# Kernel optimization log

Measured on AMD Instinct MI355X. Metric: run time of the kernel, lower is better.

The kernel has to match this reference:

```python
import jax, jax.numpy as jnp
import numpy as np

B, T, V = 256, 512, 32
CH, H, HF = 32, 64, 32  # context_hidden, hidden_size, feat-imputation hidden


def setup_inputs() -> dict:
    key = jax.random.key(0)
    ks = iter(jax.random.split(key, 48))
    rn = lambda shape, s=0.05: jax.random.normal(next(ks), shape, jnp.float32) * s
    inp = {
        'values': jax.random.normal(next(ks), (B, T, V), jnp.float32),
        'masks': (jax.random.uniform(next(ks), (B, T, V)) < 0.7).astype(jnp.float32),
        'rain_forward': jax.random.normal(next(ks), (B, T, V), jnp.float32),
        'rain_backward': jax.random.normal(next(ks), (B, T, V), jnp.float32),
        # context_mlp: Linear(3V+1, 2CH) -> ReLU -> Linear(2CH, CH)
        'cmlp_W1': rn((2 * CH, 3 * V + 1)), 'cmlp_b1': rn((2 * CH,)),
        'cmlp_W2': rn((CH, 2 * CH)), 'cmlp_b2': rn((CH,)),
        # GRUCell(3V, CH)
        'gru_Wih': rn((3 * CH, 3 * V)), 'gru_Whh': rn((3 * CH, CH)),
        'gru_bih': rn((3 * CH,)), 'gru_bhh': rn((3 * CH,)),
        # initial_hidden: Linear(2CH, 2H)
        'init_W': rn((2 * H, 2 * CH)), 'init_b': rn((2 * H,)),
        # LSTMCell(2V+2CH, H) forward / backward
        'lstmf_Wih': rn((4 * H, 2 * V + 2 * CH)), 'lstmf_Whh': rn((4 * H, H)),
        'lstmf_bih': rn((4 * H,)), 'lstmf_bhh': rn((4 * H,)),
        'lstmb_Wih': rn((4 * H, 2 * V + 2 * CH)), 'lstmb_Whh': rn((4 * H, H)),
        'lstmb_bih': rn((4 * H,)), 'lstmb_bhh': rn((4 * H,)),
        # recurrent_impute: Linear(2H, V)
        'rimp_W': rn((V, 2 * H)), 'rimp_b': rn((V,)),
        # MLPFeatureImputation
        'feat_W': rn((V, HF, V)), 'feat_b': rn((V, HF)),
        'nl1_W': rn((HF, HF)), 'nl1_b': rn((HF,)),
        'nl2_W': rn((1, HF)), 'nl2_b': rn((1,)),
        # fuse_imputations: Linear(2V, V)
        'fuse_W': rn((V, 2 * V)), 'fuse_b': rn((V,)),
        'lengths': jax.random.randint(next(ks), (B,), T // 2, T + 1).astype(jnp.int32),
    }
    return inp


def _forward(values, masks, rain_forward, rain_backward,
             cmlp_W1, cmlp_b1, cmlp_W2, cmlp_b2,
             gru_Wih, gru_Whh, gru_bih, gru_bhh,
             init_W, init_b,
             lstmf_Wih, lstmf_Whh, lstmf_bih, lstmf_bhh,
             lstmb_Wih, lstmb_Whh, lstmb_bih, lstmb_bhh,
             rimp_W, rimp_b, feat_W, feat_b,
             nl1_W, nl1_b, nl2_W, nl2_b, fuse_W, fuse_b, lengths):
    Bv, Tv, Vv = values.shape
    Hh = lstmf_Whh.shape[1]
    dt = values.dtype

    # padding mask [B,T] -> [B,T,V]
    pm_t = (jnp.arange(Tv)[None, :] < lengths[:, None]).astype(dt)
    padding_masks = jnp.broadcast_to(pm_t[:, :, None], values.shape)

    # summary statistics (faithful to the effective computation in torch forward)
    mask_sum = jnp.maximum(masks.sum(1), 1.0)
    data_means = (masks * values).sum(1) / mask_sum
    diff_sq_sum = ((values - data_means[:, None, :]) ** 2).sum(1)
    data_variance = jnp.where(mask_sum > 1, diff_sq_sum / (mask_sum - 1), 0.0)
    data_stdev = jnp.sqrt(data_variance)
    padding_sum = jnp.maximum(padding_masks.sum(1), 1.0)
    data_missing_rate = 1.0 - masks.sum(1) / padding_sum
    data_stats = jnp.concatenate(
        [lengths[:, None].astype(dt), data_means, data_stdev, data_missing_rate], axis=1)

    # last-observation shift and complement
    x_prime = jnp.concatenate([values[:, :1], values[:, :-1]], axis=1)
    x_comp = (masks * values + (1.0 - masks) * x_prime) * padding_masks

    # context MLP
    hmlp = jax.nn.relu(data_stats @ cmlp_W1.T + cmlp_b1)
    ctx_mlp = hmlp @ cmlp_W2.T + cmlp_b2  # [B,CH]

    # context GRU with per-step padding-masked hn
    gru_in = jnp.concatenate([x_comp, rain_forward, rain_backward], axis=-1)  # [B,T,3V]
    ch = gru_Whh.shape[1]

    def gru_step(carry, xt):
        h, hn = carry
        x, mt = xt
        gi = x @ gru_Wih.T + gru_bih
        gh = h @ gru_Whh.T + gru_bhh
        ir, iz, inn = jnp.split(gi, 3, axis=1)
        hr, hz, hhn = jnp.split(gh, 3, axis=1)
        r = jax.nn.sigmoid(ir + hr)
        z = jax.nn.sigmoid(iz + hz)
        n = jnp.tanh(inn + r * hhn)
        h = (1.0 - z) * n + z * h
        hn = mt[:, None] * h + (1.0 - mt[:, None]) * hn
        return (h, hn), None

    z0 = jnp.zeros((Bv, ch), dt)
    (_, ctx_rnn), _ = jax.lax.scan(gru_step, (z0, z0),
                                   (jnp.swapaxes(gru_in, 0, 1), pm_t.T))

    context_vec = jnp.concatenate([ctx_mlp, ctx_rnn], axis=1)  # [B,2CH]
    h0 = context_vec @ init_W.T + init_b   # [B,2H]
    c0 = jnp.tanh(h0)

    inputs = jnp.concatenate(
        [x_comp, masks, jnp.broadcast_to(context_vec[:, None, :], (Bv, Tv, context_vec.shape[1]))],
        axis=-1)  # [B,T,2V+2CH]
    inp_t = jnp.swapaxes(inputs, 0, 1)  # [T,B,D]

    def lstm_step(Wih, Whh, bih, bhh):
        def step(carry, x):
            h, c = carry
            g = x @ Wih.T + bih + h @ Whh.T + bhh
            i, f, gg, o = jnp.split(g, 4, axis=1)
            c = jax.nn.sigmoid(f) * c + jax.nn.sigmoid(i) * jnp.tanh(gg)
            h = jax.nn.sigmoid(o) * jnp.tanh(c)
            return (h, c), h
        return step

    h0f, h0b = h0[:, :Hh], h0[:, Hh:]
    c0f, c0b = c0[:, :Hh], c0[:, Hh:]

    # forward pass over steps 0..T-2; hiddens_forward[0] is initial state
    _, hs_f = jax.lax.scan(lstm_step(lstmf_Wih, lstmf_Whh, lstmf_bih, lstmf_bhh),
                           (h0f, c0f), inp_t[:-1])
    hiddens_forward = jnp.concatenate([h0f[None], hs_f], axis=0)  # [T,B,H]

    # backward pass over steps T-1..1; hiddens_backward[T-1] is initial state
    _, hs_b = jax.lax.scan(lstm_step(lstmb_Wih, lstmb_Whh, lstmb_bih, lstmb_bhh),
                           (h0b, c0b), jnp.flip(inp_t[1:], axis=0))
    hiddens_backward = jnp.concatenate([jnp.flip(hs_b, axis=0), h0b[None]], axis=0)

    rnn_hidden = jnp.swapaxes(
        jnp.concatenate([hiddens_forward, hiddens_backward], axis=2), 0, 1)  # [B,T,2H]
    rnn_imp = rnn_hidden @ rimp_W.T + rimp_b  # [B,T,V]

    # per-variable masked feature imputation
    m = 1.0 - jnp.eye(Vv, dtype=dt)[:, None, :]           # [V,1,V] -> zero own feature
    Wm = feat_W * m                                        # [V,HF,V]
    hid = jnp.einsum('btv,ihv->btih', x_comp, Wm) + feat_b # [B,T,V,HF]
    zh = jax.nn.relu(hid) @ nl1_W.T + nl1_b
    feat_imp = (jax.nn.relu(zh) @ nl2_W.T + nl2_b)[..., 0] # [B,T,V]

    gamma = jnp.ones_like(x_comp)
    beta = jax.nn.sigmoid(jnp.concatenate([gamma, masks], axis=-1) @ fuse_W.T + fuse_b)
    imp_fusion = beta * feat_imp + (1.0 - beta) * rnn_imp
    final_imp = masks * values + (1.0 - masks) * imp_fusion
    final_imp = jnp.where(padding_masks == 1.0, final_imp, 0.0)  # rescale()
    return final_imp


def reference(values, masks, rain_forward, rain_backward,
              cmlp_W1, cmlp_b1, cmlp_W2, cmlp_b2,
              gru_Wih, gru_Whh, gru_bih, gru_bhh,
              init_W, init_b,
              lstmf_Wih, lstmf_Whh, lstmf_bih, lstmf_bhh,
              lstmb_Wih, lstmb_Whh, lstmb_bih, lstmb_bhh,
              rimp_W, rimp_b, feat_W, feat_b,
              nl1_W, nl1_b, nl2_W, nl2_b, fuse_W, fuse_b, lengths):
    return _forward(values, masks, rain_forward, rain_backward,
                    cmlp_W1, cmlp_b1, cmlp_W2, cmlp_b2,
                    gru_Wih, gru_Whh, gru_bih, gru_bhh,
                    init_W, init_b,
                    lstmf_Wih, lstmf_Whh, lstmf_bih, lstmf_bhh,
                    lstmb_Wih, lstmb_Whh, lstmb_bih, lstmb_bhh,
                    rimp_W, rimp_b, feat_W, feat_b,
                    nl1_W, nl1_b, nl2_W, nl2_b, fuse_W, fuse_b, lengths)
```

## Files before the change

kernel.cpp:

```cpp
#include <hip/hip_runtime.h>
#include <cstddef>
#include <cstdint>

constexpr int NB = 256;
constexpr int NT = 512;
constexpr int NV = 32;

typedef _Float16 h2_t __attribute__((ext_vector_type(2)));
typedef _Float16 f16x8 __attribute__((ext_vector_type(8)));
typedef float f32x4 __attribute__((ext_vector_type(4)));

__device__ __forceinline__ float sigmoidf_(float x){ return 1.0f/(1.0f+__expf(-x)); }
__device__ __forceinline__ float tanhf_(float x){ return 1.0f - 2.0f/(__expf(2.0f*x)+1.0f); }

__device__ __forceinline__ uint32_t pack2u_(float a, float b){
  h2_t r; r.x=(_Float16)a; r.y=(_Float16)b; return __builtin_bit_cast(uint32_t, r);
}
__device__ __forceinline__ float dot2u_(uint32_t u, uint32_t w, float c){
#if __has_builtin(__builtin_amdgcn_fdot2)
  return __builtin_amdgcn_fdot2(__builtin_bit_cast(h2_t,u), __builtin_bit_cast(h2_t,w), c, false);
#else
  h2_t a=__builtin_bit_cast(h2_t,u), b=__builtin_bit_cast(h2_t,w);
  return c + (float)a.x*(float)b.x + (float)a.y*(float)b.y;
#endif
}
__device__ __forceinline__ float h2f_(unsigned short u){
  _Float16 hv = __builtin_bit_cast(_Float16, u); return (float)hv;
}
__device__ __forceinline__ unsigned short f2h_(float a){
  _Float16 hv = (_Float16)a; return __builtin_bit_cast(unsigned short, hv);
}

#define Q4(acc, Wv, Uv) { acc=dot2u_((Uv).x,(Wv).x,acc); acc=dot2u_((Uv).y,(Wv).y,acc); \
                          acc=dot2u_((Uv).z,(Wv).z,acc); acc=dot2u_((Uv).w,(Wv).w,acc); }

__global__ __launch_bounds__(256) void k_stats(
    const float* __restrict__ values, const float* __restrict__ masks,
    const int* __restrict__ lengths,
    float* __restrict__ x_comp, float* __restrict__ stats)
{
  const int b = blockIdx.x;
  const int v = threadIdx.x & 31;
  const int g = threadIdx.x >> 5;
  const int len = lengths[b];
  const float* vb = values + (size_t)b*NT*NV;
  const float* mb = masks  + (size_t)b*NT*NV;
  float* xb = x_comp + (size_t)b*NT*NV;
  float s_m=0.f, s_mv=0.f, s_v=0.f, s_v2=0.f;
  for (int t=g; t<NT; t+=8){
    float val = vb[t*NV+v];
    float m   = mb[t*NV+v];
    float xp  = (t==0) ? vb[v] : vb[(t-1)*NV+v];
    float pm  = (t<len) ? 1.0f : 0.0f;
    xb[t*NV+v] = (m*val + (1.0f-m)*xp)*pm;
    s_m += m; s_mv += m*val; s_v += val; s_v2 += val*val;
  }
  __shared__ float red[4][8][32];
  red[0][g][v]=s_m; red[1][g][v]=s_mv; red[2][g][v]=s_v; red[3][g][v]=s_v2;
  __syncthreads();
  if (g==0){
    float a0=0,a1=0,a2=0,a3=0;
    #pragma unroll
    for(int i=0;i<8;i++){ a0+=red[0][i][v]; a1+=red[1][i][v]; a2+=red[2][i][v]; a3+=red[3][i][v]; }
    float msum = fmaxf(a0, 1.0f);
    float mean = a1/msum;
    float dss  = a3 - 2.0f*mean*a2 + (float)NT*mean*mean;
    float var  = (msum > 1.0f) ? dss/(msum-1.0f) : 0.0f;
    float sd   = sqrtf(fmaxf(var, 0.0f));
    float miss = 1.0f - a0 / fmaxf((float)len, 1.0f);
    float* st = stats + b*97;
    if (v==0) st[0] = (float)len;
    st[1+v]=mean; st[33+v]=sd; st[65+v]=miss;
  }
}

__global__ __launch_bounds__(64) void k_cmlp(
    const float* __restrict__ stats,
    const float* __restrict__ W1, const float* __restrict__ b1,
    const float* __restrict__ W2, const float* __restrict__ b2,
    float* __restrict__ ctx)
{
  const int b = blockIdx.x;
  const int j = threadIdx.x;
  __shared__ float st[97];
  __shared__ float hm[64];
  for (int k=j; k<97; k+=64) st[k] = stats[b*97+k];
  __syncthreads();
  float a0=b1[j], a1=0.f, a2=0.f, a3=0.f;
  #pragma unroll
  for (int k=0; k<96; k+=4){
    a0 += st[k]*W1[j*97+k];     a1 += st[k+1]*W1[j*97+k+1];
    a2 += st[k+2]*W1[j*97+k+2]; a3 += st[k+3]*W1[j*97+k+3];
  }
  a0 += st[96]*W1[j*97+96];
  hm[j] = fmaxf((a0+a1)+(a2+a3), 0.0f);
  __syncthreads();
  if (j < 32){
    float c0_=b2[j], c1=0.f, c2=0.f, c3=0.f;
    #pragma unroll
    for (int k=0;k<64;k+=4){
      c0_ += hm[k]*W2[j*64+k];    c1 += hm[k+1]*W2[j*64+k+1];
      c2 += hm[k+2]*W2[j*64+k+2]; c3 += hm[k+3]*W2[j*64+k+3];
    }
    ctx[b*64+j] = (c0_+c1)+(c2+c3);
  }
}

__global__ __launch_bounds__(128) void k_gigru(
    const float* __restrict__ x_comp, const float* __restrict__ rain_f,
    const float* __restrict__ rain_b,
    const float* __restrict__ Wih, const float* __restrict__ bih,
    unsigned short* __restrict__ gig)
{
  __shared__ uint32_t WT[48][98];
  __shared__ __align__(16) uint32_t us[8][48];
  const int tid = threadIdx.x;
  for (int idx = tid; idx < 48*96; idx += 128){
    const int k = idx / 96, col = idx - k*96;
    WT[k][col] = pack2u_(Wih[(size_t)col*96 + 2*k], Wih[(size_t)col*96 + 2*k + 1]);
  }
  const float bias = (tid < 96) ? bih[tid] : 0.f;
  __syncthreads();
  const int NR = NB*NT;
  for (int r0 = blockIdx.x*8; r0 < NR; r0 += gridDim.x*8){
    __syncthreads();
    for (int idx = tid; idx < 8*48; idx += 128){
      const int r = idx / 48, w = idx - r*48;
      const size_t row = (size_t)r0 + r;
      const int i0 = 2*w, i1 = 2*w+1;
      const float a = (i0<32)? x_comp[row*32+i0] : (i0<64 ? rain_f[row*32+i0-32] : rain_b[row*32+i0-64]);
      const float c = (i1<32)? x_comp[row*32+i1] : (i1<64 ? rain_f[row*32+i1-32] : rain_b[row*32+i1-64]);
      us[r][w] = pack2u_(a, c);
    }
    __syncthreads();
    if (tid < 96){
      #pragma unroll
      for (int r=0;r<8;r++){
        const uint4* U = (const uint4*)us[r];
        float acc = bias;
        #pragma unroll
        for (int k4=0;k4<12;k4++){
          const uint4 u4 = U[k4];
          acc = dot2u_(u4.x, WT[4*k4][tid],   acc);
          acc = dot2u_(u4.y, WT[4*k4+1][tid], acc);
          acc = dot2u_(u4.z, WT[4*k4+2][tid], acc);
          acc = dot2u_(u4.w, WT[4*k4+3][tid], acc);
        }
        gig[((size_t)r0+r)*96 + tid] = f2h_(acc);
      }
    }
  }
}

__global__ __launch_bounds__(64,4) void k_gru(
    const unsigned short* __restrict__ gig, const int* __restrict__ lengths,
    const float* __restrict__ Whh, const float* __restrict__ bhh,
    float* __restrict__ ctx)
{
  __shared__ __align__(16) _Float16 hbuf[32];
  __shared__ __align__(16) float gbuf[96];
  const int b = blockIdx.x;
  const int l = threadIdx.x;
  const int arow = l & 15, ak = (l >> 4) * 8;
  const int crow = (l >> 4) * 4;
  f16x8 A0, A1, A2, A3, A4, A5;
  #define LDA(dst, mt) { const float* p_ = Whh + (size_t)((mt)*16 + arow)*32 + ak; \
    f16x8 t_; _Pragma("unroll") for (int e_=0;e_<8;++e_) t_[e_] = (_Float16)p_[e_]; dst = t_; }
  LDA(A0,0) LDA(A1,1) LDA(A2,2) LDA(A3,3) LDA(A4,4) LDA(A5,5)
  #undef LDA
  f32x4 bb0, bb1, bb2, bb3, bb4, bb5;
  #pragma unroll
  for (int j=0;j<4;j++){
    bb0[j] = bhh[0*16 + crow + j]; bb1[j] = bhh[1*16 + crow + j];
    bb2[j] = bhh[2*16 + crow + j]; bb3[j] = bhh[3*16 + crow + j];
    bb4[j] = bhh[4*16 + crow + j]; bb5[j] = bhh[5*16 + crow + j];
  }
  asm volatile("" ::: "memory");
  int len = lengths[b]; if (len > NT) len = NT;
  float h = 0.f;
  if (l < 32) hbuf[l] = (_Float16)0.f;
  const unsigned short* gp = gig + (size_t)b*NT*96;
  float gir=0.f, giz=0.f, gin=0.f;
  if (l < 32 && len > 0){ gir=h2f_(gp[l]); giz=h2f_(gp[32+l]); gin=h2f_(gp[64+l]); }
  __syncthreads();
  for (int t=0; t<len; ++t){
    float nr=0.f, nz=0.f, nn=0.f;
    if (l < 32 && t+1 < len){
      const unsigned short* gn = gp + (size_t)(t+1)*96;
      nr=h2f_(gn[l]); nz=h2f_(gn[32+l]); nn=h2f_(gn[64+l]);
    }
    const f16x8 bh = *(const f16x8*)&hbuf[ak];
    f32x4 a0 = bb0, a1 = bb1, a2 = bb2, a3 = bb3, a4 = bb4, a5 = bb5;
    a0 = __builtin_amdgcn_mfma_f32_16x16x32_f16(A0, bh, a0, 0, 0, 0);
    a1 = __builtin_amdgcn_mfma_f32_16x16x32_f16(A1, bh, a1, 0, 0, 0);
    a2 = __builtin_amdgcn_mfma_f32_16x16x32_f16(A2, bh, a2, 0, 0, 0);
    a3 = __builtin_amdgcn_mfma_f32_16x16x32_f16(A3, bh, a3, 0, 0, 0);
    a4 = __builtin_amdgcn_mfma_f32_16x16x32_f16(A4, bh, a4, 0, 0, 0);
    a5 = __builtin_amdgcn_mfma_f32_16x16x32_f16(A5, bh, a5, 0, 0, 0);
    if ((l & 15) == 0){
      *(f32x4*)&gbuf[0*16 + crow] = a0;
      *(f32x4*)&gbuf[1*16 + crow] = a1;
      *(f32x4*)&gbuf[2*16 + crow] = a2;
      *(f32x4*)&gbuf[3*16 + crow] = a3;
      *(f32x4*)&gbuf[4*16 + crow] = a4;
      *(f32x4*)&gbuf[5*16 + crow] = a5;
    }
    __syncthreads();
    if (l < 32){
      const float r = sigmoidf_(gir + gbuf[l]);
      const float z = sigmoidf_(giz + gbuf[32+l]);
      const float n = tanhf_(gin + r*gbuf[64+l]);
      h = (1.0f - z)*n + z*h;
      gir=nr; giz=nz; gin=nn;
      hbuf[l] = (_Float16)h;
    }
    __syncthreads();
  }
  if (l < 32) ctx[b*64 + 32 + l] = h;
}

__global__ __launch_bounds__(256) void k_init(
    const float* __restrict__ ctx,
    const float* __restrict__ initW, const float* __restrict__ initb,
    const float* __restrict__ WihF, const float* __restrict__ bihF, const float* __restrict__ bhhF,
    const float* __restrict__ WihB, const float* __restrict__ bihB, const float* __restrict__ bhhB,
    float* __restrict__ h0, float* __restrict__ c0,
    float* __restrict__ cgF, float* __restrict__ cgB,
    float* __restrict__ hidden)
{
  const int b = blockIdx.x;
  const int j = threadIdx.x;
  __shared__ __align__(16) float cv[64];
  if (j < 64) cv[j] = ctx[b*64+j];
  __syncthreads();
  {
    float4 f = {bihF[j]+bhhF[j], 0.f, 0.f, 0.f};
    float4 g = {bihB[j]+bhhB[j], 0.f, 0.f, 0.f};
    #pragma unroll
    for (int q=0;q<16;q++){
      const float4 cvv = *(const float4*)&cv[4*q];
      const float4 wf = *(const float4*)(WihF + (size_t)j*128 + 64 + 4*q);
      const float4 wb = *(const float4*)(WihB + (size_t)j*128 + 64 + 4*q);
      f.x += cvv.x*wf.x; f.y += cvv.y*wf.y; f.z += cvv.z*wf.z; f.w += cvv.w*wf.w;
      g.x += cvv.x*wb.x; g.y += cvv.y*wb.y; g.z += cvv.z*wb.z; g.w += cvv.w*wb.w;
    }
    cgF[b*256+j] = (f.x+f.y)+(f.z+f.w);
    cgB[b*256+j] = (g.x+g.y)+(g.z+g.w);
  }
  if (j < 128){
    float4 a = {initb[j], 0.f, 0.f, 0.f};
    #pragma unroll
    for (int q=0;q<16;q++){
      const float4 cvv = *(const float4*)&cv[4*q];
      const float4 w  = *(const float4*)(initW + (size_t)j*64 + 4*q);
      a.x += cvv.x*w.x; a.y += cvv.y*w.y; a.z += cvv.z*w.z; a.w += cvv.w*w.w;
    }
    float hv = (a.x+a.y)+(a.z+a.w);
    h0[b*128+j] = hv;
    c0[b*128+j] = tanhf_(hv);
    if (j < 64) hidden[(size_t)b*NT*128 + j] = hv;
    else        hidden[(size_t)b*NT*128 + (size_t)(NT-1)*128 + 64 + (j-64)] = hv;
  }
}

__global__ __launch_bounds__(256,2) void k_lstm_feat(
    const float* __restrict__ x_comp, const float* __restrict__ masks,
    const float* __restrict__ WihF, const float* __restrict__ WhhF,
    const float* __restrict__ WihB, const float* __restrict__ WhhB,
    const float* __restrict__ cgF, const float* __restrict__ cgB,
    const float* __restrict__ h0, const float* __restrict__ c0,
    const int* __restrict__ lengths,
    float* __restrict__ hidden,
    const float* __restrict__ feat_W, const float* __restrict__ feat_b,
    const float* __restrict__ nl1_W, const float* __restrict__ nl1_b,
    const float* __restrict__ nl2_W, const float* __restrict__ nl2_b,
    float* __restrict__ feat_imp)
{
  __shared__ __align__(16) _Float16 ubuf[2][64];
  __shared__ __align__(16) _Float16 hbuf[2][64];
  __shared__ __align__(16) _Float16 xbuf[16*32];
  __shared__ __align__(16) _Float16 hidb[32*16*40];
  __shared__ __align__(16) float fbl[1024];
  __shared__ float fout[16*33];
  const int tid = threadIdx.x;
  if (blockIdx.y < 2){
    const int b = blockIdx.x, dir = blockIdx.y;
    const int l = tid & 63, wv = tid >> 6;
    const int eg = wv * 16;
    const int arow = l & 15, ak = (l >> 4) * 8;
    const int rowg = l >> 4;
    const int j4 = l & 3;
    const int elem = eg + rowg*4 + j4;
    const bool writer = ((l & 15) >> 2) == 0;
    const float* Wih = dir ? WihB : WihF;
    const float* Whh = dir ? WhhB : WhhF;
    f16x8 X0a,X0b,X1a,X1b,X2a,X2b,X3a,X3b;
    f16x8 H0a,H0b,H1a,H1b,H2a,H2b,H3a,H3b;
    #define LDFRAG(dst, base, ld, row, kk) { \
      const float* p_ = (base) + (size_t)(row)*(ld) + (kk); \
      const float4 v0_ = *(const float4*)p_; const float4 v1_ = *(const float4*)(p_+4); \
      f16x8 t_; t_[0]=(_Float16)v0_.x; t_[1]=(_Float16)v0_.y; t_[2]=(_Float16)v0_.z; t_[3]=(_Float16)v0_.w; \
      t_[4]=(_Float16)v1_.x; t_[5]=(_Float16)v1_.y; t_[6]=(_Float16)v1_.z; t_[7]=(_Float16)v1_.w; dst = t_; }
    LDFRAG(X0a, Wih, 128, 0*64+eg+arow, ak)    LDFRAG(X0b, Wih, 128, 0*64+eg+arow, 32+ak)
    LDFRAG(X1a, Wih, 128, 1*64+eg+arow, ak)    LDFRAG(X1b, Wih, 128, 1*64+eg+arow, 32+ak)
    LDFRAG(X2a, Wih, 128, 2*64+eg+arow, ak)    LDFRAG(X2b, Wih, 128, 2*64+eg+arow, 32+ak)
    LDFRAG(X3a, Wih, 128, 3*64+eg+arow, ak)    LDFRAG(X3b, Wih, 128, 3*64+eg+arow, 32+ak)
    LDFRAG(H0a, Whh, 64,  0*64+eg+arow, ak)    LDFRAG(H0b, Whh, 64,  0*64+eg+arow, 32+ak)
    LDFRAG(H1a, Whh, 64,  1*64+eg+arow, ak)    LDFRAG(H1b, Whh, 64,  1*64+eg+arow, 32+ak)
    LDFRAG(H2a, Whh, 64,  2*64+eg+arow, ak)    LDFRAG(H2b, Whh, 64,  2*64+eg+arow, 32+ak)
    LDFRAG(H3a, Whh, 64,  3*64+eg+arow, ak)    LDFRAG(H3b, Whh, 64,  3*64+eg+arow, 32+ak)
    #undef LDFRAG
    const float* cgp = (dir ? cgB : cgF) + (size_t)b*256;
    const int crow = rowg * 4;
    const f32x4 cgi = *(const f32x4*)(cgp + 0*64 + eg + crow);
    const f32x4 cgf = *(const f32x4*)(cgp + 1*64 + eg + crow);
    const f32x4 cgg = *(const f32x4*)(cgp + 2*64 + eg + crow);
    const f32x4 cgo = *(const f32x4*)(cgp + 3*64 + eg + crow);
    asm volatile("" ::: "memory");
    const int len = lengths[b];
    int nsteps = NT-1;
    if (dir == 0){ int e = len-1; if (e<0) e=0; if (e<nsteps) nsteps = e; }
    const float* xc = x_comp + (size_t)b*NT*NV;
    const float* mk = masks  + (size_t)b*NT*NV;
    float* hout = hidden + (size_t)b*NT*128 + dir*64;
    float cst = c0[(size_t)b*128 + dir*64 + elem];
    if (tid < 64) hbuf[0][tid] = (_Float16)h0[(size_t)b*128 + dir*64 + tid];
    if (tid >= 64 && tid < 96 && nsteps > 0){
      const int u = tid - 64;
      const int t0 = dir ? NT-1 : 0;
      const float2 v = (u<16) ? *(const float2*)(xc + t0*NV + 2*u)
                              : *(const float2*)(mk + t0*NV + 2*(u-16));
      ubuf[0][2*u] = (_Float16)v.x; ubuf[0][2*u+1] = (_Float16)v.y;
    }
    __syncthreads();
    for (int s=0; s<nsteps; ++s){
      const int cur = s & 1;
      float2 pre = {0.f, 0.f};
      const bool dopf = (tid >= 64 && tid < 96 && s+1 < nsteps);
      if (dopf){
        const int u = tid - 64;
        const int tn = dir ? (NT-2-s) : (s+1);
        pre = (u<16) ? *(const float2*)(xc + tn*NV + 2*u)
                     : *(const float2*)(mk + tn*NV + 2*(u-16));
      }
      const f16x8 bu0 = *(const f16x8*)&ubuf[cur][ak];
      const f16x8 bu1 = *(const f16x8*)&ubuf[cur][32+ak];
      const f16x8 bh0 = *(const f16x8*)&hbuf[cur][ak];
      const f16x8 bh1 = *(const f16x8*)&hbuf[cur][32+ak];
      f32x4 ai = cgi, af = cgf, ag = cgg, ao = cgo;
      ai = __builtin_amdgcn_mfma_f32_16x16x32_f16(X0a, bu0, ai, 0, 0, 0);
      af = __builtin_amdgcn_mfma_f32_16x16x32_f16(X1a, bu0, af, 0, 0, 0);
      ag = __builtin_amdgcn_mfma_f32_16x16x32_f16(X2a, bu0, ag, 0, 0, 0);
      ao = __builtin_amdgcn_mfma_f32_16x16x32_f16(X3a, bu0, ao, 0, 0, 0);
      ai = __builtin_amdgcn_mfma_f32_16x16x32_f16(X0b, bu1, ai, 0, 0, 0);
      af = __builtin_amdgcn_mfma_f32_16x16x32_f16(X1b, bu1, af, 0, 0, 0);
      ag = __builtin_amdgcn_mfma_f32_16x16x32_f16(X2b, bu1, ag, 0, 0, 0);
      ao = __builtin_amdgcn_mfma_f32_16x16x32_f16(X3b, bu1, ao, 0, 0, 0);
      ai = __builtin_amdgcn_mfma_f32_16x16x32_f16(H0a, bh0, ai, 0, 0, 0);
      af = __builtin_amdgcn_mfma_f32_16x16x32_f16(H1a, bh0, af, 0, 0, 0);
      ag = __builtin_amdgcn_mfma_f32_16x16x32_f16(H2a, bh0, ag, 0, 0, 0);
      ao = __builtin_amdgcn_mfma_f32_16x16x32_f16(H3a, bh0, ao, 0, 0, 0);
      ai = __builtin_amdgcn_mfma_f32_16x16x32_f16(H0b, bh1, ai, 0, 0, 0);
      af = __builtin_amdgcn_mfma_f32_16x16x32_f16(H1b, bh1, af, 0, 0, 0);
      ag = __builtin_amdgcn_mfma_f32_16x16x32_f16(H2b, bh1, ag, 0, 0, 0);
      ao = __builtin_amdgcn_mfma_f32_16x16x32_f16(H3b, bh1, ao, 0, 0, 0);
      const float gi = ai[j4], gf = af[j4], gg = ag[j4], go = ao[j4];
      cst = sigmoidf_(gf)*cst + sigmoidf_(gi)*tanhf_(gg);
      const float hh = sigmoidf_(go)*tanhf_(cst);
      if (writer){
        hbuf[cur^1][elem] = (_Float16)hh;
        const int outt = dir ? (NT-2-s) : (s+1);
        hout[(size_t)outt*128 + elem] = hh;
      }
      if (dopf){
        const int u = tid - 64;
        ubuf[cur^1][2*u]   = (_Float16)pre.x;
        ubuf[cur^1][2*u+1] = (_Float16)pre.y;
      }
      __syncthreads();
    }
    return;
  }
  {
    const int l = tid & 63, wv = tid >> 6;
    const int fr = l >> 4, fc = l & 15;
    const int ak = fr * 8;
    f16x8 WA[16];
    #pragma unroll
    for (int q=0;q<16;q++){
      const int m_ = (wv*16 + q)*16 + fc;
      const int i_ = m_ >> 5;
      const float* s_ = feat_W + (size_t)m_*32 + ak;
      f16x8 t_;
      #pragma unroll
      for (int e_=0; e_<8; ++e_){
        float w_ = s_[e_];
        if (ak + e_ == i_) w_ = 0.f;
        t_[e_] = (_Float16)w_;
      }
      WA[q] = t_;
    }
    f16x8 NA0, NA1;
    {
      f16x8 t0, t1;
      #pragma unroll
      for (int e=0;e<8;e++){
        t0[e] = (_Float16)nl1_W[(fc)*32 + ak + e];
        t1[e] = (_Float16)nl1_W[(16 + fc)*32 + ak + e];
      }
      NA0 = t0; NA1 = t1;
    }
    f32x4 n1b0, n1b1;
    float n2w0[4], n2w1[4];
    #pragma unroll
    for (int j=0;j<4;j++){
      n1b0[j] = nl1_b[fr*4+j];
      n1b1[j] = nl1_b[16 + fr*4+j];
      n2w0[j] = nl2_W[fr*4+j];
      n2w1[j] = nl2_W[16 + fr*4+j];
    }
    const float n2b = nl2_b[0];
    for (int idx = tid; idx < 1024; idx += 256) fbl[idx] = feat_b[idx];
    asm volatile("" ::: "memory");
    const int NG = (NB*NT)/16;
    for (int g = blockIdx.x; g < NG; g += 256){
      const size_t r0 = (size_t)g*16;
      __syncthreads();
      {
        const int n0 = tid >> 4, v2 = (tid & 15)*2;
        const float2 xv = *(const float2*)&x_comp[(r0+n0)*32 + v2];
        xbuf[n0*32+v2]   = (_Float16)xv.x;
        xbuf[n0*32+v2+1] = (_Float16)xv.y;
      }
      __syncthreads();
      const f16x8 xB = *(const f16x8*)&xbuf[fc*32 + ak];
      #pragma unroll
      for (int q=0;q<16;q++){
        const int mt = wv*16 + q;
        f32x4 acc = {0.f,0.f,0.f,0.f};
        acc = __builtin_amdgcn_mfma_f32_16x16x32_f16(WA[q], xB, acc, 0, 0, 0);
        const int mbase = mt*16 + fr*4;
        const f32x4 fb4 = *(const f32x4*)&fbl[mbase];
        #pragma unroll
        for (int jj=0;jj<4;jj+=2){
          const int m0_ = mbase + jj;
          const int i_ = m0_ >> 5, h_ = m0_ & 31;
          const float v0_ = fmaxf(acc[jj]   + fb4[jj],   0.f);
          const float v1_ = fmaxf(acc[jj+1] + fb4[jj+1], 0.f);
          h2_t p; p.x = (_Float16)v0_; p.y = (_Float16)v1_;
          *(h2_t*)&hidb[(i_*16+fc)*40 + h_] = p;
        }
      }
      __syncthreads();
      float outv[8];
      #pragma unroll
      for (int q=0;q<8;q++){
        const int nt = wv*8 + q;
        const f16x8 hB = *(const f16x8*)&hidb[(nt*16+fc)*40 + ak];
        f32x4 z0 = n1b0, z1 = n1b1;
        z0 = __builtin_amdgcn_mfma_f32_16x16x32_f16(NA0, hB, z0, 0, 0, 0);
        z1 = __builtin_amdgcn_mfma_f32_16x16x32_f16(NA1, hB, z1, 0, 0, 0);
        float s = 0.f;
        #pragma unroll
        for (int j=0;j<4;j++){
          s += fmaxf(z0[j], 0.f)*n2w0[j];
          s += fmaxf(z1[j], 0.f)*n2w1[j];
        }
        s += __shfl_xor(s, 16);
        s += __shfl_xor(s, 32);
        outv[q] = s;
      }
      if (fr == 0){
        #pragma unroll
        for (int q=0;q<8;q++) fout[fc*33 + wv*8 + q] = outv[q] + n2b;
      }
      __syncthreads();
      feat_imp[r0*32 + tid]       = fout[(tid>>5)*33 + (tid&31)];
      feat_imp[r0*32 + 256 + tid] = fout[((tid+256)>>5)*33 + (tid&31)];
    }
  }
}

__global__ __launch_bounds__(512) void k_final(
    const float* __restrict__ values, const float* __restrict__ masks,
    const float* __restrict__ feat_imp, const float* __restrict__ hidden,
    const float* __restrict__ rimp_W, const float* __restrict__ rimp_b,
    const float* __restrict__ fuse_W, const float* __restrict__ fuse_b,
    const int* __restrict__ lengths, float* __restrict__ out)
{
  const int tid = threadIdx.x;
  const int v = tid & 31;
  const int grp = (tid >> 5) & 7;
  const int half = tid >> 8;
  __shared__ uint32_t rpT[64][32];
  __shared__ __align__(16) uint32_t hrowp[8][64];
  __shared__ float rpart[8][32];
  __shared__ float bpart[8][32];
  for (int idx = tid; idx < 64*32; idx += 512){
    const int k = idx >> 5, vv = idx & 31;
    rpT[k][vv] = pack2u_(rimp_W[(size_t)vv*128 + 2*k], rimp_W[(size_t)vv*128 + 2*k+1]);
  }
  const float4* F4 = (const float4*)(fuse_W + (size_t)v*64 + 32);
  float fconst = 0.f;
  if (!half){
    fconst = fuse_b[v];
    #pragma unroll
    for (int q=0;q<8;q++){
      const float4 fw = *(const float4*)(fuse_W + (size_t)v*64 + 4*q);
      fconst += (fw.x+fw.y)+(fw.z+fw.w);
    }
  }
  const float rbias = rimp_b[v];
  __syncthreads();
  const int NOCT = (NB*NT)/8;
  for (int oc = blockIdx.x; oc < NOCT; oc += gridDim.x){
    const size_t base = (size_t)oc*8;
    __syncthreads();
    if (tid < 256){
      const float4 hv = ((const float4*)(hidden + base*128))[tid];
      const int row = tid >> 5;
      const int w0 = (tid & 31) << 1;
      hrowp[row][w0]   = pack2u_(hv.x, hv.y);
      hrowp[row][w0+1] = pack2u_(hv.z, hv.w);
    }
    __syncthreads();
    const size_t r = base + grp;
    float a = half ? 0.f : rbias;
    {
      const uint4* hp4 = (const uint4*)&hrowp[grp][half*32];
      #pragma unroll
      for (int c4=0;c4<8;c4++){
        const uint4 H = hp4[c4];
        a = dot2u_(H.x, rpT[half*32 + 4*c4][v],     a);
        a = dot2u_(H.y, rpT[half*32 + 4*c4 + 1][v], a);
        a = dot2u_(H.z, rpT[half*32 + 4*c4 + 2][v], a);
        a = dot2u_(H.w, rpT[half*32 + 4*c4 + 3][v], a);
      }
    }
    if (half){
      rpart[grp][v] = a;
      const float* mrow = masks + r*32;
      float m0=0,m1=0,m2=0,m3=0;
      #pragma unroll
      for (int q=0;q<8;q++){
        const float4 mv = *(const float4*)(mrow + 4*q);
        const float4 fv = F4[q];
        m0 = fmaf(mv.x, fv.x, m0); m1 = fmaf(mv.y, fv.y, m1);
        m2 = fmaf(mv.z, fv.z, m2); m3 = fmaf(mv.w, fv.w, m3);
      }
      bpart[grp][v] = (m0+m1)+(m2+m3);
    }
    __syncthreads();
    if (!half){
      const int bb = (int)(r >> 9);
      const int t  = (int)(r & 511);
      const int len = lengths[bb];
      const float rimp = a + rpart[grp][v];
      const float beta = sigmoidf_(fconst + bpart[grp][v]);
      const float fi = feat_imp[r*32+v];
      const float m  = masks[r*32+v];
      const float val= values[r*32+v];
      const float fz = beta*fi + (1.0f-beta)*rimp;
      const float o = m*val + (1.0f-m)*fz;
      out[r*32+v] = (t < len) ? o : 0.0f;
    }
  }
}

extern "C" void kernel_launch(void* const* d_in, const int* in_sizes, int n_in,
                              void* d_out, int out_size, void* d_ws, size_t ws_size,
                              hipStream_t stream) {
  const float* values   = (const float*)d_in[0];
  const float* masks    = (const float*)d_in[1];
  const float* rain_f   = (const float*)d_in[2];
  const float* rain_b   = (const float*)d_in[3];
  const float* cmlp_W1  = (const float*)d_in[4];
  const float* cmlp_b1  = (const float*)d_in[5];
  const float* cmlp_W2  = (const float*)d_in[6];
  const float* cmlp_b2  = (const float*)d_in[7];
  const float* gru_Wih  = (const float*)d_in[8];
  const float* gru_Whh  = (const float*)d_in[9];
  const float* gru_bih  = (const float*)d_in[10];
  const float* gru_bhh  = (const float*)d_in[11];
  const float* init_W   = (const float*)d_in[12];
  const float* init_b   = (const float*)d_in[13];
  const float* lstmf_Wih= (const float*)d_in[14];
  const float* lstmf_Whh= (const float*)d_in[15];
  const float* lstmf_bih= (const float*)d_in[16];
  const float* lstmf_bhh= (const float*)d_in[17];
  const float* lstmb_Wih= (const float*)d_in[18];
  const float* lstmb_Whh= (const float*)d_in[19];
  const float* lstmb_bih= (const float*)d_in[20];
  const float* lstmb_bhh= (const float*)d_in[21];
  const float* rimp_W   = (const float*)d_in[22];
  const float* rimp_b   = (const float*)d_in[23];
  const float* feat_W   = (const float*)d_in[24];
  const float* feat_b   = (const float*)d_in[25];
  const float* nl1_W    = (const float*)d_in[26];
  const float* nl1_b    = (const float*)d_in[27];
  const float* nl2_W    = (const float*)d_in[28];
  const float* nl2_b    = (const float*)d_in[29];
  const float* fuse_W   = (const float*)d_in[30];
  const float* fuse_b   = (const float*)d_in[31];
  const int*   lengths  = (const int*)d_in[32];
  float* out = (float*)d_out;

  float* ws       = (float*)d_ws;
  float* x_comp   = ws;
  float* stats    = x_comp + (size_t)NB*NT*NV;
  float* ctx      = stats + NB*97;
  float* h0       = ctx + NB*64;
  float* c0      = h0 + NB*128;
  float* cgF      = c0 + NB*128;
  float* cgB      = cgF + NB*256;
  float* hidden   = cgB + NB*256;
  float* feat_imp = hidden + (size_t)NB*NT*128;
  unsigned short* gig = (unsigned short*)(feat_imp + (size_t)NB*NT*NV);

  k_stats<<<NB, 256, 0, stream>>>(values, masks, lengths, x_comp, stats);
  k_gigru<<<1024, 128, 0, stream>>>(x_comp, rain_f, rain_b, gru_Wih, gru_bih, gig);
  k_cmlp<<<NB, 64, 0, stream>>>(stats, cmlp_W1, cmlp_b1, cmlp_W2, cmlp_b2, ctx);
  k_gru<<<NB, 64, 0, stream>>>(gig, lengths, gru_Whh, gru_bhh, ctx);
  k_init<<<NB, 256, 0, stream>>>(ctx, init_W, init_b,
                                 lstmf_Wih, lstmf_bih, lstmf_bhh,
                                 lstmb_Wih, lstmb_bih, lstmb_bhh,
                                 h0, c0, cgF, cgB, hidden);
  dim3 lgrid(NB, 3);
  k_lstm_feat<<<lgrid, 256, 0, stream>>>(x_comp, masks,
                                         lstmf_Wih, lstmf_Whh, lstmb_Wih, lstmb_Whh,
                                         cgF, cgB, h0, c0, lengths, hidden,
                                         feat_W, feat_b, nl1_W, nl1_b, nl2_W, nl2_b, feat_imp);
  k_final<<<2048, 512, 0, stream>>>(values, masks, feat_imp, hidden,
                                    rimp_W, rimp_b, fuse_W, fuse_b, lengths, out);
}
```

Before: 1.078 ms.

## Compute GRU gates directly from MFMA registers with double-buffered hidden state

The GRU recurrence now evaluates the gate nonlinearities in every lane straight from the MFMA accumulator registers, instead of staging gate pre-activations through shared memory. The hidden state is double-buffered, which cuts the per-step barriers from two to one. Each lane carries two hidden elements and redundantly loads the input-gate values, trading some extra ALU work and loads for less shared-memory traffic and synchronisation on the serial critical path. The input-projection kernel's grid is also doubled.

```diff
diff --git a/kernel.cpp b/kernel.cpp
--- a/kernel.cpp
+++ b/kernel.cpp
@@ -157,12 +157,14 @@
     const float* __restrict__ Whh, const float* __restrict__ bhh,
     float* __restrict__ ctx)
 {
-  __shared__ __align__(16) _Float16 hbuf[32];
-  __shared__ __align__(16) float gbuf[96];
+  __shared__ __align__(16) _Float16 hbuf[2][32];
   const int b = blockIdx.x;
   const int l = threadIdx.x;
   const int arow = l & 15, ak = (l >> 4) * 8;
-  const int crow = (l >> 4) * 4;
+  const int rg = l >> 4, j4 = l & 3;
+  const int crow = rg * 4;
+  const int e0 = crow + j4, e1 = 16 + e0;
+  const bool writer = ((l & 15) >> 2) == 0;
   f16x8 A0, A1, A2, A3, A4, A5;
   #define LDA(dst, mt) { const float* p_ = Whh + (size_t)((mt)*16 + arow)*32 + ak; \
     f16x8 t_; _Pragma("unroll") for (int e_=0;e_<8;++e_) t_[e_] = (_Float16)p_[e_]; dst = t_; }
@@ -177,19 +179,24 @@
   }
   asm volatile("" ::: "memory");
   int len = lengths[b]; if (len > NT) len = NT;
-  float h = 0.f;
-  if (l < 32) hbuf[l] = (_Float16)0.f;
+  float h0v = 0.f, h1v = 0.f;
+  if (l < 32) hbuf[0][l] = (_Float16)0.f;
   const unsigned short* gp = gig + (size_t)b*NT*96;
-  float gir=0.f, giz=0.f, gin=0.f;
-  if (l < 32 && len > 0){ gir=h2f_(gp[l]); giz=h2f_(gp[32+l]); gin=h2f_(gp[64+l]); }
+  float gir0=0.f, giz0=0.f, gin0=0.f, gir1=0.f, giz1=0.f, gin1=0.f;
+  if (len > 0){
+    gir0 = h2f_(gp[e0]); giz0 = h2f_(gp[32+e0]); gin0 = h2f_(gp[64+e0]);
+    gir1 = h2f_(gp[e1]); giz1 = h2f_(gp[32+e1]); gin1 = h2f_(gp[64+e1]);
+  }
   __syncthreads();
   for (int t=0; t<len; ++t){
-    float nr=0.f, nz=0.f, nn=0.f;
-    if (l < 32 && t+1 < len){
+    const int cur = t & 1;
+    float nr0=0.f,nz0=0.f,nn0=0.f, nr1=0.f,nz1=0.f,nn1=0.f;
+    if (t+1 < len){
       const unsigned short* gn = gp + (size_t)(t+1)*96;
-      nr=h2f_(gn[l]); nz=h2f_(gn[32+l]); nn=h2f_(gn[64+l]);
-    }
-    const f16x8 bh = *(const f16x8*)&hbuf[ak];
+      nr0 = h2f_(gn[e0]); nz0 = h2f_(gn[32+e0]); nn0 = h2f_(gn[64+e0]);
+      nr1 = h2f_(gn[e1]); nz1 = h2f_(gn[32+e1]); nn1 = h2f_(gn[64+e1]);
+    }
+    const f16x8 bh = *(const f16x8*)&hbuf[cur][ak];
     f32x4 a0 = bb0, a1 = bb1, a2 = bb2, a3 = bb3, a4 = bb4, a5 = bb5;
     a0 = __builtin_amdgcn_mfma_f32_16x16x32_f16(A0, bh, a0, 0, 0, 0);
     a1 = __builtin_amdgcn_mfma_f32_16x16x32_f16(A1, bh, a1, 0, 0, 0);
@@ -197,26 +204,26 @@
     a3 = __builtin_amdgcn_mfma_f32_16x16x32_f16(A3, bh, a3, 0, 0, 0);
     a4 = __builtin_amdgcn_mfma_f32_16x16x32_f16(A4, bh, a4, 0, 0, 0);
     a5 = __builtin_amdgcn_mfma_f32_16x16x32_f16(A5, bh, a5, 0, 0, 0);
-    if ((l & 15) == 0){
-      *(f32x4*)&gbuf[0*16 + crow] = a0;
-      *(f32x4*)&gbuf[1*16 + crow] = a1;
-      *(f32x4*)&gbuf[2*16 + crow] = a2;
-      *(f32x4*)&gbuf[3*16 + crow] = a3;
-      *(f32x4*)&gbuf[4*16 + crow] = a4;
-      *(f32x4*)&gbuf[5*16 + crow] = a5;
-    }
+    const float r0 = sigmoidf_(gir0 + a0[j4]);
+    const float z0 = sigmoidf_(giz0 + a2[j4]);
+    const float n0 = tanhf_(gin0 + r0*a4[j4]);
+    h0v = (1.0f - z0)*n0 + z0*h0v;
+    const float r1 = sigmoidf_(gir1 + a1[j4]);
+    const float z1 = sigmoidf_(giz1 + a3[j4]);
+    const float n1 = tanhf_(gin1 + r1*a5[j4]);
+    h1v = (1.0f - z1)*n1 + z1*h1v;
+    if (writer){
+      hbuf[cur^1][e0] = (_Float16)h0v;
+      hbuf[cur^1][e1] = (_Float16)h1v;
+    }
+    gir0=nr0; giz0=nz0; gin0=nn0;
+    gir1=nr1; giz1=nz1; gin1=nn1;
     __syncthreads();
-    if (l < 32){
-      const float r = sigmoidf_(gir + gbuf[l]);
-      const float z = sigmoidf_(giz + gbuf[32+l]);
-      const float n = tanhf_(gin + r*gbuf[64+l]);
-      h = (1.0f - z)*n + z*h;
-      gir=nr; giz=nz; gin=nn;
-      hbuf[l] = (_Float16)h;
-    }
-    __syncthreads();
-  }
-  if (l < 32) ctx[b*64 + 32 + l] = h;
+  }
+  if (writer){
+    ctx[b*64 + 32 + e0] = h0v;
+    ctx[b*64 + 32 + e1] = h1v;
+  }
 }
 
 __global__ __launch_bounds__(256) void k_init(
@@ -618,7 +625,7 @@
   unsigned short* gig = (unsigned short*)(feat_imp + (size_t)NB*NT*NV);
 
   k_stats<<<NB, 256, 0, stream>>>(values, masks, lengths, x_comp, stats);
-  k_gigru<<<1024, 128, 0, stream>>>(x_comp, rain_f, rain_b, gru_Wih, gru_bih, gig);
+  k_gigru<<<2048, 128, 0, stream>>>(x_comp, rain_f, rain_b, gru_Wih, gru_bih, gig);
   k_cmlp<<<NB, 64, 0, stream>>>(stats, cmlp_W1, cmlp_b1, cmlp_W2, cmlp_b2, ctx);
   k_gru<<<NB, 64, 0, stream>>>(gig, lengths, gru_Whh, gru_bhh, ctx);
   k_init<<<NB, 256, 0, stream>>>(ctx, init_W, init_b,
```

New measurement: 1.089 ms. Within noise of the previous version (+1.0%).
